# Performance work log

Measured on AMD Instinct MI355X. Metric: run time of the kernel, lower is better.

Reference implementation:

```python
import jax, jax.numpy as jnp
import numpy as np

D = 512
H = 4
HD = D // H
FF = 4 * D
B = 512
T = 128
EMA_K = 128
LOC_K = 4
DECAY = 0.9
STEP = 0.5 / np.sqrt(128 / 32)  # 0.25
EPS = 1e-5


def layernorm(x, g, b):
    mu = jnp.mean(x, axis=-1, keepdims=True)
    var = jnp.mean(jnp.square(x - mu), axis=-1, keepdims=True)
    return (x - mu) * jax.lax.rsqrt(var + EPS) * g + b


def dwconv_causal(x, w):
    # x: (B,T,D), w: (D,K); torch Conv1d(groups=D, padding=K-1) sliced to [:T]
    K = w.shape[1]
    xt = jnp.transpose(x, (0, 2, 1))  # (B,D,T)
    y = jax.lax.conv_general_dilated(
        xt, w[:, None, :], window_strides=(1,), padding=[(K - 1, 0)],
        feature_group_count=x.shape[-1], dimension_numbers=('NCT', 'OIT', 'NCT'))
    return jnp.transpose(y, (0, 2, 1))


def rope(qk, cos, sin):
    # qk: (B,H,T,HD)
    x1, x2 = jnp.split(qk, 2, axis=-1)
    rot = jnp.concatenate([-x2, x1], axis=-1)
    return qk * cos + rot * sin


def setup_inputs() -> dict:
    key = jax.random.key(0)
    ks = jax.random.split(key, 24)
    s = 0.02
    inp = {
        'parallel_repr': jax.random.normal(ks[0], (B, T, D), jnp.float32),
        'sequential_state': jax.random.normal(ks[1], (B, D), jnp.float32),
        'q_w': jax.random.normal(ks[2], (D, D), jnp.float32) * s,
        'q_b': jnp.zeros((D,), jnp.float32),
        'k_w': jax.random.normal(ks[3], (D, D), jnp.float32) * s,
        'k_b': jnp.zeros((D,), jnp.float32),
        'v_w': jax.random.normal(ks[4], (D, D), jnp.float32) * s,
        'v_b': jnp.zeros((D,), jnp.float32),
        'o_w': jax.random.normal(ks[5], (D, D), jnp.float32) * s,
        'o_b': jnp.zeros((D,), jnp.float32),
        'local_w': jax.random.normal(ks[6], (D, LOC_K), jnp.float32) * 0.1,
        'local_b': jax.random.normal(ks[7], (D,), jnp.float32) * 0.1,
        'delta_w': jax.random.normal(ks[8], (3 * D, D), jnp.float32) * s,
        'delta_b': jnp.zeros((D,), jnp.float32),
        'gate_w': jax.random.normal(ks[9], (3 * D, D), jnp.float32) * s,
        'gate_b': jnp.zeros((D,), jnp.float32),
        'dn_g': jnp.ones((D,), jnp.float32), 'dn_b': jnp.zeros((D,), jnp.float32),
        'ln1_g': jnp.ones((D,), jnp.float32), 'ln1_b': jnp.zeros((D,), jnp.float32),
        'ln2_g': jnp.ones((D,), jnp.float32), 'ln2_b': jnp.zeros((D,), jnp.float32),
        'ln3_g': jnp.ones((D,), jnp.float32), 'ln3_b': jnp.zeros((D,), jnp.float32),
        'ln4_g': jnp.ones((D,), jnp.float32), 'ln4_b': jnp.zeros((D,), jnp.float32),
        'seq_w': jax.random.normal(ks[10], (D, D), jnp.float32) * s,
        'seq_b': jnp.zeros((D,), jnp.float32),
        'ffn_w1': jax.random.normal(ks[11], (D, FF), jnp.float32) * s,
        'ffn_b1': jnp.zeros((FF,), jnp.float32),
        'ffn_w2': jax.random.normal(ks[12], (FF, D), jnp.float32) * s,
        'ffn_b2': jnp.zeros((D,), jnp.float32),
    }
    # EMA kernel: coefficient (1-d)*d^lag on x[t-lag]; stored flipped as in torch
    ema = (1.0 - DECAY) * DECAY ** jnp.arange(EMA_K, dtype=jnp.float32)
    inp['ema_w'] = jnp.broadcast_to(ema[::-1][None, :], (D, EMA_K))
    return inp


def reference(parallel_repr, sequential_state, q_w, q_b, k_w, k_b, v_w, v_b,
              o_w, o_b, local_w, local_b, delta_w, delta_b, gate_w, gate_b,
              dn_g, dn_b, ln1_g, ln1_b, ln2_g, ln2_b, ln3_g, ln3_b, ln4_g, ln4_b,
              seq_w, seq_b, ffn_w1, ffn_b1, ffn_w2, ffn_b2, ema_w):
    x = parallel_repr
    Bb, Tt, Dd = x.shape
    # --- RoPE causal attention ---
    inv_freq = 1.0 / (10000.0 ** (jnp.arange(0, HD, 2, dtype=jnp.float32) / HD))
    t = jnp.arange(Tt, dtype=jnp.float32)
    freqs = jnp.outer(t, inv_freq)                      # (T, HD/2)
    emb = jnp.concatenate([freqs, freqs], axis=-1)      # (T, HD)
    cos = jnp.cos(emb)[None, None]
    sin = jnp.sin(emb)[None, None]
    def heads(y):
        return jnp.transpose(y.reshape(Bb, Tt, H, HD), (0, 2, 1, 3))
    q = rope(heads(x @ q_w + q_b), cos, sin)
    k = rope(heads(x @ k_w + k_b), cos, sin)
    v = heads(x @ v_w + v_b)
    scores = jnp.einsum('bhtd,bhsd->bhts', q, k) / np.sqrt(HD)
    causal = jnp.tril(jnp.ones((Tt, Tt), dtype=bool))
    scores = jnp.where(causal, scores, jnp.float32(-1e9))
    attn = jax.nn.softmax(scores, axis=-1)
    attn_out = jnp.einsum('bhts,bhsd->bhtd', attn, v)
    attn_out = jnp.transpose(attn_out, (0, 2, 1, 3)).reshape(Bb, Tt, Dd)
    attn_out = attn_out @ o_w + o_b
    x1 = layernorm(x + attn_out, ln1_g, ln1_b)
    # --- depthwise causal convs ---
    local_hist = dwconv_causal(x1, local_w) + local_b
    global_sum = dwconv_causal(x1, ema_w)
    combined = jnp.concatenate([x1, local_hist, global_sum], axis=-1)  # (B,T,3D)
    deltas = jax.nn.sigmoid(combined @ gate_w + gate_b) * jnp.tanh(combined @ delta_w + delta_b)
    deltas = layernorm(deltas, dn_g, dn_b)
    acc = jnp.cumsum(deltas, axis=1) * STEP
    states = layernorm(sequential_state[:, None, :] + acc, ln3_g, ln3_b)
    seq_guidance = states @ seq_w + seq_b
    ffn_in = x1 + 0.3 * seq_guidance
    h = jax.nn.gelu(ffn_in @ ffn_w1 + ffn_b1, approximate=False)
    ffn_out = h @ ffn_w2 + ffn_b2
    out = layernorm(x1 + ffn_out, ln2_g, ln2_b)
    final_state = layernorm(states[:, -1, :], ln4_g, ln4_b)
    return out, final_state
```

## Files before the change

### kernel.cpp

```cpp
#include <hip/hip_runtime.h>
#include <cstddef>
#include <cstdint>

#define BB   512
#define TT   128
#define DD   512
#define HH   4
#define HDIM 128
#define FFD  2048
#define NROWS (BB * TT)
#define SLOT ((size_t)NROWS * DD)

typedef unsigned short u16;
typedef __bf16 bf16x8 __attribute__((ext_vector_type(8)));
typedef float  f32x4  __attribute__((ext_vector_type(4)));

__device__ __forceinline__ u16 f2b(float x) {
    union { float f; unsigned u; } v; v.f = x;
    unsigned r = v.u + 0x7FFFu + ((v.u >> 16) & 1u);
    return (u16)(r >> 16);
}
__device__ __forceinline__ float b2f(u16 u) {
    union { unsigned u; float f; } v; v.u = (unsigned)u << 16; return v.f;
}

__device__ __forceinline__ void glds16(const void* g, void* l) {
    __builtin_amdgcn_global_load_lds(
        (const __attribute__((address_space(1))) void*)g,
        (__attribute__((address_space(3))) void*)l, 16, 0, 0);
}

template<int MODE>
__global__ __launch_bounds__(256)
void gemm_bf16(const u16* __restrict__ A, const u16* __restrict__ BT,
               const float* __restrict__ bias, void* __restrict__ Cout, int ldc,
               const float* __restrict__ addsrc, int K, int M)
{
    __shared__ u16 As[128 * 32];
    __shared__ u16 Bs[128 * 32];
    __shared__ u16 Ct[(MODE == 5) ? 128 * 128 : 8];
    const int tid = threadIdx.x;
    const int gx  = gridDim.x;
    const int nwg = gx * gridDim.y;
    int orig = blockIdx.y * gx + blockIdx.x;
    if ((nwg & 7) == 0) orig = (orig & 7) * (nwg >> 3) + (orig >> 3);
    const int row0 = (orig / gx) * 128;
    const int col0 = (orig % gx) * 128;

    const int lane = tid & 63;
    const int w    = tid >> 6;
    const int wr   = (w >> 1) * 64;
    const int wc   = (w & 1) * 64;
    const int fr   = lane & 15;
    const int kg   = (lane >> 4) * 8;

    f32x4 acc[4][4];
#pragma unroll
    for (int m = 0; m < 4; ++m)
#pragma unroll
        for (int n = 0; n < 4; ++n) acc[m][n] = (f32x4){0.f, 0.f, 0.f, 0.f};

    const int srow = tid >> 2;
    const int skb  = (tid & 3) * 8;
    const u16* Ag = A  + (size_t)(row0 + srow) * K + skb;
    const u16* Bg = BT + (size_t)(col0 + srow) * K + skb;
    u16* AsP = &As[srow * 32 + skb];
    u16* BsP = &Bs[srow * 32 + skb];

    for (int k0 = 0; k0 < K; k0 += 32) {
        glds16(Ag + k0,                  AsP);
        glds16(Ag + (size_t)64 * K + k0, AsP + 64 * 32);
        glds16(Bg + k0,                  BsP);
        glds16(Bg + (size_t)64 * K + k0, BsP + 64 * 32);
        __syncthreads();
        bf16x8 af[4], bfr[4];
#pragma unroll
        for (int m = 0; m < 4; ++m)
            af[m] = *reinterpret_cast<const bf16x8*>(&As[(wr + m * 16 + fr) * 32 + kg]);
#pragma unroll
        for (int n = 0; n < 4; ++n)
            bfr[n] = *reinterpret_cast<const bf16x8*>(&Bs[(wc + n * 16 + fr) * 32 + kg]);
#pragma unroll
        for (int m = 0; m < 4; ++m)
#pragma unroll
            for (int n = 0; n < 4; ++n)
                acc[m][n] = __builtin_amdgcn_mfma_f32_16x16x32_bf16(af[m], bfr[n], acc[m][n], 0, 0, 0);
        __syncthreads();
    }

    if constexpr (MODE == 5) {
#pragma unroll
        for (int m = 0; m < 4; ++m)
#pragma unroll
            for (int j = 0; j < 4; ++j) {
                const int tl = wr + m * 16 + (lane >> 4) * 4 + j;
#pragma unroll
                for (int n = 0; n < 4; ++n) {
                    const int dc = wc + n * 16 + fr;
                    float v = acc[m][n][j] + bias[col0 + dc];
                    *(u16*)((char*)Ct + dc * 256 + ((tl * 2) ^ ((dc & 7) << 4))) = f2b(v);
                }
            }
        __syncthreads();
        u16* dst = (u16*)Cout + (((size_t)(row0 >> 7) * (M >> 7) + (col0 >> 7)) << 14);
#pragma unroll
        for (int i = 0; i < 8; ++i)
            *(uint4*)(dst + (size_t)(i * 256 + tid) * 8) =
                *(const uint4*)((char*)Ct + (size_t)(i * 256 + tid) * 16);
    } else {
#pragma unroll
        for (int m = 0; m < 4; ++m) {
#pragma unroll
            for (int j = 0; j < 4; ++j) {
                const int r = row0 + wr + m * 16 + (lane >> 4) * 4 + j;
#pragma unroll
                for (int n = 0; n < 4; ++n) {
                    const int c = col0 + wc + n * 16 + fr;
                    float v = acc[m][n][j] + bias[c];
                    if constexpr (MODE == 0) {
                        ((float*)Cout)[(size_t)r * ldc + c] = v;
                    } else if constexpr (MODE == 2) {
                        ((u16*)Cout)[(size_t)r * ldc + c] =
                            f2b(addsrc[(size_t)r * M + c] + 0.3f * v);
                    } else if constexpr (MODE == 3) {
                        float gv = 0.5f * v * (1.f + erff(v * 0.70710678118654752f));
                        ((u16*)Cout)[(size_t)r * ldc + c] = f2b(gv);
                    } else {
                        ((u16*)Cout)[(size_t)r * ldc + c] = f2b(v);
                    }
                }
            }
        }
    }
}

__global__ __launch_bounds__(256)
void wtrans_kernel(const float* __restrict__ W, u16* __restrict__ WT, int K, int M)
{
    __shared__ float t[32][33];
    const int m0 = blockIdx.x * 32;
    const int k0 = blockIdx.y * 32;
    const int tx = threadIdx.x;
    const int ty = threadIdx.y;
#pragma unroll
    for (int i = 0; i < 4; ++i) {
        int k = ty * 4 + i;
        t[k][tx] = W[(size_t)(k0 + k) * M + m0 + tx];
    }
    __syncthreads();
#pragma unroll
    for (int i = 0; i < 4; ++i) {
        int m = ty * 4 + i;
        WT[(size_t)(m0 + m) * K + k0 + tx] = f2b(t[tx][m]);
    }
}

__global__ void cast_f2b_kernel(const float* __restrict__ in, u16* __restrict__ out, size_t n4)
{
    size_t i = (size_t)blockIdx.x * blockDim.x + threadIdx.x;
    if (i >= n4) return;
    float4 v = reinterpret_cast<const float4*>(in)[i];
    union { u16 u[4]; uint2 d; } p;
    p.u[0] = f2b(v.x); p.u[1] = f2b(v.y); p.u[2] = f2b(v.z); p.u[3] = f2b(v.w);
    reinterpret_cast<uint2*>(out)[i] = p.d;
}

__global__ void rope_table_kernel(float* __restrict__ tabc, float* __restrict__ tabs)
{
    int idx = blockIdx.x * blockDim.x + threadIdx.x;
    if (idx >= TT * 64) return;
    int t = idx >> 6, j = idx & 63;
    float invf = expf(-(float)j * (9.210340371976184f / 64.f));
    float ang  = (float)t * invf;
    tabc[idx] = cosf(ang);
    tabs[idx] = sinf(ang);
}

__global__ __launch_bounds__(256)
void attn_mfma_kernel(const u16* __restrict__ Qg, const u16* __restrict__ Kg,
                      const u16* __restrict__ VTg, u16* __restrict__ Og,
                      const float* __restrict__ tabc, const float* __restrict__ tabs)
{
    __shared__ u16 SA[128 * 128];
    __shared__ u16 SB[128 * 128];
    const int h = blockIdx.x, b = blockIdx.y;
    const int tid  = threadIdx.x;
    const int lane = tid & 63;
    const int w    = tid >> 6;
    const int fr   = lane & 15;
    const int kq   = lane >> 4;
    const size_t base = ((size_t)(b * TT)) * DD + (size_t)h * HDIM;

    {
        const int tg = tid >> 4;
        const int dg = tid & 15;
        const int j0 = (dg & 7) * 8;
        const bool hi = (dg & 8) != 0;
        for (int r = 0; r < 8; ++r) {
            const int t = r * 16 + tg;
            uint4 qv = *(const uint4*)(Qg + base + (size_t)t * DD + dg * 8);
            uint4 kv = *(const uint4*)(Kg + base + (size_t)t * DD + dg * 8);
            unsigned qa[4] = {qv.x, qv.y, qv.z, qv.w};
            unsigned ka[4] = {kv.x, kv.y, kv.z, kv.w};
            unsigned qb[4], kb[4];
#pragma unroll
            for (int i = 0; i < 4; ++i) {
                qb[i] = __shfl_xor((int)qa[i], 8);
                kb[i] = __shfl_xor((int)ka[i], 8);
            }
            const float* cp = tabc + t * 64 + j0;
            const float* sp = tabs + t * 64 + j0;
            u16 oq[8], ok[8];
#pragma unroll
            for (int e = 0; e < 8; ++e) {
                float fq = b2f((u16)(qa[e >> 1] >> ((e & 1) * 16)));
                float gq = b2f((u16)(qb[e >> 1] >> ((e & 1) * 16)));
                float fk = b2f((u16)(ka[e >> 1] >> ((e & 1) * 16)));
                float gk = b2f((u16)(kb[e >> 1] >> ((e & 1) * 16)));
                float c = cp[e], s = sp[e];
                oq[e] = f2b(hi ? fq * c + gq * s : fq * c - gq * s);
                ok[e] = f2b(hi ? fk * c + gk * s : fk * c - gk * s);
            }
            const int cb = (dg * 16) ^ ((t & 7) << 4);
            *(uint4*)((char*)SA + t * 256 + cb) = *(const uint4*)oq;
            *(uint4*)((char*)SB + t * 256 + cb) = *(const uint4*)ok;
        }
    }
    __syncthreads();

    f32x4 acc[2][8];
#pragma unroll
    for (int m = 0; m < 2; ++m)
#pragma unroll
        for (int n = 0; n < 8; ++n) acc[m][n] = (f32x4){0.f, 0.f, 0.f, 0.f};

    for (int k0 = 0; k0 < 128; k0 += 32) {
        const int cb = (k0 + kq * 8) * 2;
        bf16x8 af[2];
#pragma unroll
        for (int m = 0; m < 2; ++m) {
            const int row = w * 32 + m * 16 + fr;
            af[m] = *(const bf16x8*)((char*)SA + row * 256 + (cb ^ ((row & 7) << 4)));
        }
#pragma unroll
        for (int n = 0; n < 8; ++n) {
            const int row = n * 16 + fr;
            bf16x8 bf = *(const bf16x8*)((char*)SB + row * 256 + (cb ^ ((row & 7) << 4)));
            acc[0][n] = __builtin_amdgcn_mfma_f32_16x16x32_bf16(af[0], bf, acc[0][n], 0, 0, 0);
            acc[1][n] = __builtin_amdgcn_mfma_f32_16x16x32_bf16(af[1], bf, acc[1][n], 0, 0, 0);
        }
    }
    __syncthreads();

    {
        const u16* vsrc = VTg + ((size_t)(b * HH + h) << 14);
#pragma unroll
        for (int i = 0; i < 8; ++i)
            glds16(vsrc + (size_t)(i * 256 + tid) * 8,
                   SB + (size_t)(i * 256 + tid) * 8);
    }

    const float SC = 0.08838834764831845f;
#pragma unroll
    for (int m = 0; m < 2; ++m) {
#pragma unroll
        for (int j = 0; j < 4; ++j) {
            const int t = w * 32 + m * 16 + kq * 4 + j;
            float mx = -3.0e38f;
#pragma unroll
            for (int n = 0; n < 8; ++n) {
                const int s = n * 16 + fr;
                float v = acc[m][n][j];
                v = (s <= t) ? v * SC : -3.0e38f;
                acc[m][n][j] = v;
                mx = fmaxf(mx, v);
            }
            mx = fmaxf(mx, __shfl_xor(mx, 1));
            mx = fmaxf(mx, __shfl_xor(mx, 2));
            mx = fmaxf(mx, __shfl_xor(mx, 4));
            mx = fmaxf(mx, __shfl_xor(mx, 8));
            float sum = 0.f;
#pragma unroll
            for (int n = 0; n < 8; ++n) {
                float e = __expf(acc[m][n][j] - mx);
                acc[m][n][j] = e; sum += e;
            }
            sum += __shfl_xor(sum, 1); sum += __shfl_xor(sum, 2);
            sum += __shfl_xor(sum, 4); sum += __shfl_xor(sum, 8);
            const float inv = 1.f / sum;
#pragma unroll
            for (int n = 0; n < 8; ++n) {
                const int s = n * 16 + fr;
                *(u16*)((char*)SA + t * 256 + ((s * 2) ^ ((t & 7) << 4))) =
                    f2b(acc[m][n][j] * inv);
            }
        }
    }
    __syncthreads();

    f32x4 oa[2][8];
#pragma unroll
    for (int m = 0; m < 2; ++m)
#pragma unroll
        for (int n = 0; n < 8; ++n) oa[m][n] = (f32x4){0.f, 0.f, 0.f, 0.f};

    for (int k0 = 0; k0 < 128; k0 += 32) {
        const int cb = (k0 + kq * 8) * 2;
        bf16x8 pa[2];
#pragma unroll
        for (int m = 0; m < 2; ++m) {
            const int row = w * 32 + m * 16 + fr;
            pa[m] = *(const bf16x8*)((char*)SA + row * 256 + (cb ^ ((row & 7) << 4)));
        }
#pragma unroll
        for (int n = 0; n < 8; ++n) {
            const int row = n * 16 + fr;
            bf16x8 vb = *(const bf16x8*)((char*)SB + row * 256 + (cb ^ ((row & 7) << 4)));
            oa[0][n] = __builtin_amdgcn_mfma_f32_16x16x32_bf16(pa[0], vb, oa[0][n], 0, 0, 0);
            oa[1][n] = __builtin_amdgcn_mfma_f32_16x16x32_bf16(pa[1], vb, oa[1][n], 0, 0, 0);
        }
    }

#pragma unroll
    for (int m = 0; m < 2; ++m)
#pragma unroll
        for (int j = 0; j < 4; ++j) {
            const int t = w * 32 + m * 16 + kq * 4 + j;
            u16* orow = Og + base + (size_t)t * DD;
#pragma unroll
            for (int n = 0; n < 8; ++n)
                orow[n * 16 + fr] = f2b(oa[m][n][j]);
        }
}

__global__ __launch_bounds__(256)
void ln_kernel(const float* __restrict__ a, size_t a_stride,
               const float* __restrict__ badd, int b_mode,
               const float* __restrict__ g, const float* __restrict__ bb,
               float* __restrict__ out, size_t out_stride,
               u16* __restrict__ out2, size_t out2_stride)
{
    const int row = blockIdx.x;
    const int tid = threadIdx.x;
    const float* ap = a + (size_t)row * a_stride;
    float v0 = ap[tid];
    float v1 = ap[tid + 256];
    if (b_mode == 1) {
        const float* bp = badd + (size_t)row * DD;
        v0 += bp[tid]; v1 += bp[tid + 256];
    } else if (b_mode == 2) {
        const float* bp = badd + (size_t)(row / TT) * DD;
        v0 += bp[tid]; v1 += bp[tid + 256];
    }
    float s  = v0 + v1;
    float ss = v0 * v0 + v1 * v1;
#pragma unroll
    for (int off = 1; off < 64; off <<= 1) {
        s  += __shfl_xor(s, off);
        ss += __shfl_xor(ss, off);
    }
    __shared__ float sm1[4], sm2[4];
    const int wid = tid >> 6;
    if ((tid & 63) == 0) { sm1[wid] = s; sm2[wid] = ss; }
    __syncthreads();
    s  = sm1[0] + sm1[1] + sm1[2] + sm1[3];
    ss = sm2[0] + sm2[1] + sm2[2] + sm2[3];
    const float mu  = s * (1.f / DD);
    const float var = ss * (1.f / DD) - mu * mu;
    const float r   = rsqrtf(var + 1e-5f);
    const float o0 = (v0 - mu) * r * g[tid]       + bb[tid];
    const float o1 = (v1 - mu) * r * g[tid + 256] + bb[tid + 256];
    if (out) {
        float* op = out + (size_t)row * out_stride;
        op[tid] = o0; op[tid + 256] = o1;
    }
    if (out2) {
        u16* op2 = out2 + (size_t)row * out2_stride;
        op2[tid] = f2b(o0); op2[tid + 256] = f2b(o1);
    }
}

__global__ void local_conv_kernel(const float* __restrict__ x, const float* __restrict__ w,
                                  const float* __restrict__ b, u16* __restrict__ y, size_t n)
{
    size_t idx = (size_t)blockIdx.x * blockDim.x + threadIdx.x;
    if (idx >= n) return;
    int d = idx & (DD - 1);
    int t = (int)(idx >> 9) & (TT - 1);
    size_t row = idx >> 9;
    float acc = b[d];
#pragma unroll
    for (int kk = 0; kk < 4; ++kk) {
        int ts = t - 3 + kk;
        if (ts >= 0) acc += w[d * 4 + kk] * x[idx - (size_t)(3 - kk) * DD];
    }
    y[row * 1536 + d] = f2b(acc);
}

__global__ void ema_scan_kernel(const float* __restrict__ x, u16* __restrict__ y)
{
    int idx = blockIdx.x * blockDim.x + threadIdx.x;
    if (idx >= BB * DD) return;
    int b = idx >> 9, d = idx & (DD - 1);
    const float* xp = x + (size_t)b * TT * DD + d;
    u16* yp = y + (size_t)(b * TT) * 1536 + d;
    float acc = 0.f;
    for (int t = 0; t < TT; ++t) {
        acc = 0.9f * acc + 0.1f * xp[(size_t)t * DD];
        yp[(size_t)t * 1536] = f2b(acc);
    }
}

__global__ void cumsum_kernel(const float* __restrict__ x, float* __restrict__ y)
{
    int idx = blockIdx.x * blockDim.x + threadIdx.x;
    if (idx >= BB * DD) return;
    int b = idx >> 9, d = idx & (DD - 1);
    const float* xp = x + (size_t)b * TT * DD + d;
    float* yp = y + (size_t)b * TT * DD + d;
    float acc = 0.f;
    for (int t = 0; t < TT; ++t) {
        acc += xp[(size_t)t * DD];
        yp[(size_t)t * DD] = acc * 0.25f;
    }
}

__global__ void deltas_act_kernel(float* __restrict__ gate, const float* __restrict__ delta,
                                  size_t n)
{
    size_t idx = (size_t)blockIdx.x * blockDim.x + threadIdx.x;
    if (idx >= n) return;
    float gv = gate[idx];
    float dv = delta[idx];
    gate[idx] = (1.f / (1.f + expf(-gv))) * tanhf(dv);
}

extern "C" void kernel_launch(void* const* d_in, const int* in_sizes, int n_in,
                              void* d_out, int out_size, void* d_ws, size_t ws_size,
                              hipStream_t stream)
{
    const float* x       = (const float*)d_in[0];
    const float* seqst   = (const float*)d_in[1];
    const float* q_w     = (const float*)d_in[2];
    const float* q_b     = (const float*)d_in[3];
    const float* k_w     = (const float*)d_in[4];
    const float* k_b     = (const float*)d_in[5];
    const float* v_w     = (const float*)d_in[6];
    const float* v_b     = (const float*)d_in[7];
    const float* o_w     = (const float*)d_in[8];
    const float* o_b     = (const float*)d_in[9];
    const float* local_w = (const float*)d_in[10];
    const float* local_b = (const float*)d_in[11];
    const float* delta_w = (const float*)d_in[12];
    const float* delta_b = (const float*)d_in[13];
    const float* gate_w  = (const float*)d_in[14];
    const float* gate_b  = (const float*)d_in[15];
    const float* dn_g    = (const float*)d_in[16];
    const float* dn_b    = (const float*)d_in[17];
    const float* ln1_g   = (const float*)d_in[18];
    const float* ln1_b   = (const float*)d_in[19];
    const float* ln2_g   = (const float*)d_in[20];
    const float* ln2_b   = (const float*)d_in[21];
    const float* ln3_g   = (const float*)d_in[22];
    const float* ln3_b   = (const float*)d_in[23];
    const float* ln4_g   = (const float*)d_in[24];
    const float* ln4_b   = (const float*)d_in[25];
    const float* seq_w   = (const float*)d_in[26];
    const float* seq_b   = (const float*)d_in[27];
    const float* ffn_w1  = (const float*)d_in[28];
    const float* ffn_b1  = (const float*)d_in[29];
    const float* ffn_w2  = (const float*)d_in[30];
    const float* ffn_b2  = (const float*)d_in[31];
    (void)in_sizes; (void)n_in; (void)out_size; (void)ws_size;

    float* out = (float*)d_out;
    char*  ws  = (char*)d_ws;
    const size_t MB = (size_t)1 << 20;

    u16*   xb   = (u16*)(ws + 0);
    u16*   Qb   = (u16*)(ws + 64 * MB);
    u16*   Kb   = (u16*)(ws + 128 * MB);
    u16*   VTb  = (u16*)(ws + 192 * MB);
    u16*   attnb = (u16*)(ws + 256 * MB);
    u16*   WSa  = (u16*)(ws + 448 * MB);
    u16*   WSb  = (u16*)(ws + 456 * MB);
    float* Oo   = (float*)(ws + 0);
    u16*   Cb   = (u16*)(ws + 128 * MB);
    float* Dl   = (float*)(ws + 320 * MB);
    float* Sst  = Dl;
    u16*   statesb = (u16*)(ws + 0);
    u16*   ffn_inb = (u16*)(ws + 64 * MB);
    u16*   hb      = (u16*)(ws + 128 * MB);
    float* Fo      = (float*)(ws + 0);

    float* X1     = out;
    float* tabc   = out + SLOT;
    float* tabs   = tabc + TT * 64;
    float* fstate = out + SLOT;

    auto wtrans = [&](const float* W, u16* WT, int K, int M) {
        wtrans_kernel<<<dim3(M / 32, K / 32), dim3(32, 8), 0, stream>>>(W, WT, K, M);
    };

    const size_t NE = (size_t)NROWS * DD;
    const int EB = 256;
    const int NBLK = (int)((NE + EB - 1) / EB);

    rope_table_kernel<<<(TT * 64 + 255) / 256, 256, 0, stream>>>(tabc, tabs);
    cast_f2b_kernel<<<(unsigned)((NE / 4 + 255) / 256), 256, 0, stream>>>(x, xb, NE / 4);

    wtrans(q_w, WSa, DD, DD);
    gemm_bf16<4><<<dim3(4, 512), 256, 0, stream>>>(xb, WSa, q_b, Qb, DD, nullptr, DD, DD);
    wtrans(k_w, WSa, DD, DD);
    gemm_bf16<4><<<dim3(4, 512), 256, 0, stream>>>(xb, WSa, k_b, Kb, DD, nullptr, DD, DD);
    wtrans(v_w, WSa, DD, DD);
    gemm_bf16<5><<<dim3(4, 512), 256, 0, stream>>>(xb, WSa, v_b, VTb, 0, nullptr, DD, DD);

    attn_mfma_kernel<<<dim3(HH, BB), 256, 0, stream>>>(Qb, Kb, VTb, attnb, tabc, tabs);

    wtrans(o_w, WSa, DD, DD);
    gemm_bf16<0><<<dim3(4, 512), 256, 0, stream>>>(attnb, WSa, o_b, Oo, DD, nullptr, DD, DD);

    ln_kernel<<<NROWS, 256, 0, stream>>>(x, DD, Oo, 1, ln1_g, ln1_b, X1, DD, Cb, 1536);

    local_conv_kernel<<<NBLK, EB, 0, stream>>>(X1, local_w, local_b, Cb + 512, NE);
    ema_scan_kernel<<<(BB * DD + 255) / 256, 256, 0, stream>>>(X1, Cb + 1024);

    wtrans(gate_w, WSa, 3 * DD, DD);
    gemm_bf16<0><<<dim3(4, 512), 256, 0, stream>>>(Cb, WSa, gate_b, Oo, DD, nullptr, 3 * DD, DD);
    wtrans(delta_w, WSa, 3 * DD, DD);
    gemm_bf16<0><<<dim3(4, 512), 256, 0, stream>>>(Cb, WSa, delta_b, Dl, DD, nullptr, 3 * DD, DD);

    deltas_act_kernel<<<NBLK, EB, 0, stream>>>(Oo, Dl, NE);
    ln_kernel<<<NROWS, 256, 0, stream>>>(Oo, DD, nullptr, 0, dn_g, dn_b, Oo, DD, nullptr, 0);

    cumsum_kernel<<<(BB * DD + 255) / 256, 256, 0, stream>>>(Oo, Sst);
    ln_kernel<<<NROWS, 256, 0, stream>>>(Sst, DD, seqst, 2, ln3_g, ln3_b, Sst, DD, statesb, DD);

    ln_kernel<<<BB, 256, 0, stream>>>(Sst + (size_t)(TT - 1) * DD, (size_t)TT * DD,
                                      nullptr, 0, ln4_g, ln4_b, fstate, DD, nullptr, 0);

    wtrans(seq_w, WSa, DD, DD);
    gemm_bf16<2><<<dim3(4, 512), 256, 0, stream>>>(statesb, WSa, seq_b, ffn_inb, DD, X1, DD, DD);

    wtrans(ffn_w1, WSa, DD, FFD);
    wtrans(ffn_w2, WSb, FFD, DD);
    gemm_bf16<3><<<dim3(16, 512), 256, 0, stream>>>(ffn_inb, WSa, ffn_b1, hb, FFD, nullptr, DD, FFD);
    gemm_bf16<0><<<dim3(4, 512), 256, 0, stream>>>(hb, WSb, ffn_b2, Fo, DD, nullptr, FFD, DD);

    ln_kernel<<<NROWS, 256, 0, stream>>>(X1, DD, Fo, 1, ln2_g, ln2_b, out, DD, nullptr, 0);
}
```

Before: 1.976 ms.

## Fuse QKV and gate/delta GEMMs, double-buffer GEMM, chain LN/conv/scan kernels

```diff
diff --git a/kernel.cpp b/kernel.cpp
--- a/kernel.cpp
+++ b/kernel.cpp
@@ -23,7 +23,12 @@
 __device__ __forceinline__ float b2f(u16 u) {
     union { unsigned u; float f; } v; v.u = (unsigned)u << 16; return v.f;
 }
-
+__device__ __forceinline__ float fast_gelu(float v) {
+    float t = v * (0.7978845608028654f + 0.0356774081f * v * v);
+    float e = __expf(2.f * t);
+    float th = 1.f - 2.f / (e + 1.f);
+    return 0.5f * v * (1.f + th);
+}
 __device__ __forceinline__ void glds16(const void* g, void* l) {
     __builtin_amdgcn_global_load_lds(
         (const __attribute__((address_space(1))) void*)g,
@@ -34,11 +39,10 @@
 __global__ __launch_bounds__(256)
 void gemm_bf16(const u16* __restrict__ A, const u16* __restrict__ BT,
                const float* __restrict__ bias, void* __restrict__ Cout, int ldc,
-               const float* __restrict__ addsrc, int K, int M)
-{
-    __shared__ u16 As[128 * 32];
-    __shared__ u16 Bs[128 * 32];
-    __shared__ u16 Ct[(MODE == 5) ? 128 * 128 : 8];
+               const float* __restrict__ addsrc, void* __restrict__ aux,
+               int K, int M)
+{
+    __shared__ u16 smem[16384];
     const int tid = threadIdx.x;
     const int gx  = gridDim.x;
     const int nwg = gx * gridDim.y;
@@ -64,15 +68,30 @@
     const int skb  = (tid & 3) * 8;
     const u16* Ag = A  + (size_t)(row0 + srow) * K + skb;
     const u16* Bg = BT + (size_t)(col0 + srow) * K + skb;
-    u16* AsP = &As[srow * 32 + skb];
-    u16* BsP = &Bs[srow * 32 + skb];
-
-    for (int k0 = 0; k0 < K; k0 += 32) {
-        glds16(Ag + k0,                  AsP);
-        glds16(Ag + (size_t)64 * K + k0, AsP + 64 * 32);
-        glds16(Bg + k0,                  BsP);
-        glds16(Bg + (size_t)64 * K + k0, BsP + 64 * 32);
+    const int soff = srow * 32 + skb;
+
+    auto stage = [&](int kt, int buf) {
+        const int ko = kt * 32;
+        u16* as = smem + buf * 8192 + soff;
+        u16* bs = smem + buf * 8192 + 4096 + soff;
+        glds16(Ag + ko,                  as);
+        glds16(Ag + (size_t)64 * K + ko, as + 2048);
+        glds16(Bg + ko,                  bs);
+        glds16(Bg + (size_t)64 * K + ko, bs + 2048);
+    };
+
+    const int nk = K >> 5;
+    stage(0, 0);
+    for (int k = 0; k < nk; ++k) {
+        if (k + 1 < nk) {
+            stage(k + 1, (k + 1) & 1);
+            asm volatile("s_waitcnt vmcnt(4)" ::: "memory");
+        } else {
+            asm volatile("s_waitcnt vmcnt(0)" ::: "memory");
+        }
         __syncthreads();
+        const u16* As = smem + (k & 1) * 8192;
+        const u16* Bs = As + 4096;
         bf16x8 af[4], bfr[4];
 #pragma unroll
         for (int m = 0; m < 4; ++m)
@@ -88,25 +107,58 @@
         __syncthreads();
     }
 
-    if constexpr (MODE == 5) {
+    if constexpr (MODE == 7) {
+        if (col0 >= 1024) {
+#pragma unroll
+            for (int m = 0; m < 4; ++m)
+#pragma unroll
+                for (int j = 0; j < 4; ++j) {
+                    const int tl = wr + m * 16 + (lane >> 4) * 4 + j;
+#pragma unroll
+                    for (int n = 0; n < 4; ++n) {
+                        const int dc = wc + n * 16 + fr;
+                        float v = acc[m][n][j] + bias[col0 + dc];
+                        *(u16*)((char*)smem + dc * 256 + ((tl * 2) ^ ((dc & 7) << 4))) = f2b(v);
+                    }
+                }
+            __syncthreads();
+            u16* dst = (u16*)aux + ((size_t)((row0 >> 7) * 4 + ((col0 - 1024) >> 7)) << 14);
+#pragma unroll
+            for (int i = 0; i < 8; ++i)
+                *(uint4*)(dst + (size_t)(i * 256 + tid) * 8) =
+                    *(const uint4*)((char*)smem + (size_t)(i * 256 + tid) * 16);
+        } else {
+#pragma unroll
+            for (int m = 0; m < 4; ++m)
+#pragma unroll
+                for (int j = 0; j < 4; ++j) {
+                    const int r = row0 + wr + m * 16 + (lane >> 4) * 4 + j;
+#pragma unroll
+                    for (int n = 0; n < 4; ++n) {
+                        const int c = col0 + wc + n * 16 + fr;
+                        ((u16*)Cout)[(size_t)r * 1024 + c] = f2b(acc[m][n][j] + bias[c]);
+                    }
+                }
+        }
+    } else if constexpr (MODE == 6) {
 #pragma unroll
         for (int m = 0; m < 4; ++m)
 #pragma unroll
             for (int j = 0; j < 4; ++j) {
-                const int tl = wr + m * 16 + (lane >> 4) * 4 + j;
+                const int r = row0 + wr + m * 16 + (lane >> 4) * 4 + j;
 #pragma unroll
                 for (int n = 0; n < 4; ++n) {
-                    const int dc = wc + n * 16 + fr;
-                    float v = acc[m][n][j] + bias[col0 + dc];
-                    *(u16*)((char*)Ct + dc * 256 + ((tl * 2) ^ ((dc & 7) << 4))) = f2b(v);
+                    const int c = col0 + wc + n * 16 + fr;
+                    float v = acc[m][n][j] + bias[c];
+                    float p = __shfl_xor(v, 1);
+                    if ((fr & 1) == 0) {
+                        float sg = 1.f / (1.f + __expf(-v));
+                        float e  = __expf(2.f * p);
+                        float th = 1.f - 2.f / (e + 1.f);
+                        ((u16*)Cout)[(size_t)r * ldc + (c >> 1)] = f2b(sg * th);
+                    }
                 }
             }
-        __syncthreads();
-        u16* dst = (u16*)Cout + (((size_t)(row0 >> 7) * (M >> 7) + (col0 >> 7)) << 14);
-#pragma unroll
-        for (int i = 0; i < 8; ++i)
-            *(uint4*)(dst + (size_t)(i * 256 + tid) * 8) =
-                *(const uint4*)((char*)Ct + (size_t)(i * 256 + tid) * 16);
     } else {
 #pragma unroll
         for (int m = 0; m < 4; ++m) {
@@ -123,8 +175,7 @@
                         ((u16*)Cout)[(size_t)r * ldc + c] =
                             f2b(addsrc[(size_t)r * M + c] + 0.3f * v);
                     } else if constexpr (MODE == 3) {
-                        float gv = 0.5f * v * (1.f + erff(v * 0.70710678118654752f));
-                        ((u16*)Cout)[(size_t)r * ldc + c] = f2b(gv);
+                        ((u16*)Cout)[(size_t)r * ldc + c] = f2b(fast_gelu(v));
                     } else {
                         ((u16*)Cout)[(size_t)r * ldc + c] = f2b(v);
                     }
@@ -135,7 +186,8 @@
 }
 
 __global__ __launch_bounds__(256)
-void wtrans_kernel(const float* __restrict__ W, u16* __restrict__ WT, int K, int M)
+void wtrans_kernel(const float* __restrict__ W, u16* __restrict__ WT, int K, int M,
+                   int rmul, int roff)
 {
     __shared__ float t[32][33];
     const int m0 = blockIdx.x * 32;
@@ -151,7 +203,7 @@
 #pragma unroll
     for (int i = 0; i < 4; ++i) {
         int m = ty * 4 + i;
-        WT[(size_t)(m0 + m) * K + k0 + tx] = f2b(t[tx][m]);
+        WT[(size_t)((m0 + m) * rmul + roff) * K + k0 + tx] = f2b(t[tx][m]);
     }
 }
 
@@ -176,9 +228,19 @@
     tabs[idx] = sinf(ang);
 }
 
+__global__ void bias_build_kernel(const float* qb, const float* kb, const float* vb,
+                                  const float* gb, const float* db,
+                                  float* qkvb, float* gdb)
+{
+    int i = blockIdx.x * blockDim.x + threadIdx.x;
+    if (i >= 512) return;
+    qkvb[i] = qb[i]; qkvb[512 + i] = kb[i]; qkvb[1024 + i] = vb[i];
+    gdb[2 * i] = gb[i]; gdb[2 * i + 1] = db[i];
+}
+
 __global__ __launch_bounds__(256)
-void attn_mfma_kernel(const u16* __restrict__ Qg, const u16* __restrict__ Kg,
-                      const u16* __restrict__ VTg, u16* __restrict__ Og,
+void attn_mfma_kernel(const u16* __restrict__ QKg, const u16* __restrict__ VTg,
+                      u16* __restrict__ Og,
                       const float* __restrict__ tabc, const float* __restrict__ tabs)
 {
     __shared__ u16 SA[128 * 128];
@@ -189,7 +251,8 @@
     const int w    = tid >> 6;
     const int fr   = lane & 15;
     const int kq   = lane >> 4;
-    const size_t base = ((size_t)(b * TT)) * DD + (size_t)h * HDIM;
+    const size_t baseq = ((size_t)(b * TT)) * 1024 + (size_t)h * HDIM;
+    const size_t baseo = ((size_t)(b * TT)) * DD + (size_t)h * HDIM;
 
     {
         const int tg = tid >> 4;
@@ -198,8 +261,8 @@
         const bool hi = (dg & 8) != 0;
         for (int r = 0; r < 8; ++r) {
             const int t = r * 16 + tg;
-            uint4 qv = *(const uint4*)(Qg + base + (size_t)t * DD + dg * 8);
-            uint4 kv = *(const uint4*)(Kg + base + (size_t)t * DD + dg * 8);
+            uint4 qv = *(const uint4*)(QKg + baseq + (size_t)t * 1024 + dg * 8);
+            uint4 kv = *(const uint4*)(QKg + baseq + 512 + (size_t)t * 1024 + dg * 8);
             unsigned qa[4] = {qv.x, qv.y, qv.z, qv.w};
             unsigned ka[4] = {kv.x, kv.y, kv.z, kv.w};
             unsigned qb[4], kb[4];
@@ -326,32 +389,112 @@
 #pragma unroll
         for (int j = 0; j < 4; ++j) {
             const int t = w * 32 + m * 16 + kq * 4 + j;
-            u16* orow = Og + base + (size_t)t * DD;
+            u16* orow = Og + baseo + (size_t)t * DD;
 #pragma unroll
             for (int n = 0; n < 8; ++n)
                 orow[n * 16 + fr] = f2b(oa[m][n][j]);
         }
 }
 
+__device__ __forceinline__ float2 blk_red512(float v, float (*red)[2], int tid)
+{
+    float s = v, ss = v * v;
+#pragma unroll
+    for (int off = 1; off < 64; off <<= 1) {
+        s  += __shfl_xor(s, off);
+        ss += __shfl_xor(ss, off);
+    }
+    if ((tid & 63) == 0) { red[tid >> 6][0] = s; red[tid >> 6][1] = ss; }
+    __syncthreads();
+    float S = 0.f, SS = 0.f;
+#pragma unroll
+    for (int w = 0; w < 8; ++w) { S += red[w][0]; SS += red[w][1]; }
+    return make_float2(S, SS);
+}
+
+__global__ __launch_bounds__(512)
+void ln1_chain_kernel(const float* __restrict__ x, const u16* __restrict__ oo,
+                      const float* __restrict__ g, const float* __restrict__ bb,
+                      const float* __restrict__ lw, const float* __restrict__ lb,
+                      float* __restrict__ X1, u16* __restrict__ Cb)
+{
+    __shared__ float red[2][8][2];
+    const int b = blockIdx.x, d = threadIdx.x;
+    const float g_ = g[d], b_ = bb[d];
+    const float w0 = lw[d * 4 + 0], w1 = lw[d * 4 + 1],
+                w2 = lw[d * 4 + 2], w3 = lw[d * 4 + 3];
+    const float lb_ = lb[d];
+    const size_t rb = (size_t)b * TT;
+    float h1 = 0.f, h2 = 0.f, h3 = 0.f, ema = 0.f;
+    float v = x[(rb + 0) * DD + d] + b2f(oo[(rb + 0) * DD + d]);
+    for (int t = 0; t < TT; ++t) {
+        const int tn = (t < TT - 1) ? t + 1 : t;
+        float vn = x[(rb + tn) * DD + d] + b2f(oo[(rb + tn) * DD + d]);
+        float2 r = blk_red512(v, red[t & 1], d);
+        float mu  = r.x * (1.f / DD);
+        float var = r.y * (1.f / DD) - mu * mu;
+        float x1v = (v - mu) * rsqrtf(var + 1e-5f) * g_ + b_;
+        const size_t row = rb + t;
+        X1[row * DD + d] = x1v;
+        u16* crow = Cb + row * 1536;
+        crow[d] = f2b(x1v);
+        crow[512 + d]  = f2b(lb_ + w3 * x1v + w2 * h1 + w1 * h2 + w0 * h3);
+        ema = 0.9f * ema + 0.1f * x1v;
+        crow[1024 + d] = f2b(ema);
+        h3 = h2; h2 = h1; h1 = x1v;
+        v = vn;
+    }
+}
+
+__global__ __launch_bounds__(512)
+void state_chain_kernel(const u16* __restrict__ deltasB, const float* __restrict__ seqst,
+                        const float* __restrict__ dng, const float* __restrict__ dnb,
+                        const float* __restrict__ g3, const float* __restrict__ b3,
+                        const float* __restrict__ g4, const float* __restrict__ b4,
+                        u16* __restrict__ statesb, float* __restrict__ fstate)
+{
+    __shared__ float red[2][8][2];
+    const int b = blockIdx.x, d = threadIdx.x;
+    const float gd_ = dng[d], bd_ = dnb[d], g3_ = g3[d], b3_ = b3[d];
+    const float seq = seqst[(size_t)b * DD + d];
+    const size_t rb = (size_t)b * TT;
+    float cum = 0.f;
+    float v = b2f(deltasB[(rb + 0) * DD + d]);
+    for (int t = 0; t < TT; ++t) {
+        const int tn = (t < TT - 1) ? t + 1 : t;
+        float vn = b2f(deltasB[(rb + tn) * DD + d]);
+        float2 r0 = blk_red512(v, red[0], d);
+        float mu  = r0.x * (1.f / DD);
+        float var = r0.y * (1.f / DD) - mu * mu;
+        float nd  = (v - mu) * rsqrtf(var + 1e-5f) * gd_ + bd_;
+        cum += nd;
+        float sv = seq + cum * 0.25f;
+        float2 r1 = blk_red512(sv, red[1], d);
+        mu  = r1.x * (1.f / DD);
+        var = r1.y * (1.f / DD) - mu * mu;
+        float o = (sv - mu) * rsqrtf(var + 1e-5f) * g3_ + b3_;
+        statesb[(rb + t) * DD + d] = f2b(o);
+        if (t == TT - 1) {
+            float2 r2 = blk_red512(o, red[0], d);
+            float mu4  = r2.x * (1.f / DD);
+            float var4 = r2.y * (1.f / DD) - mu4 * mu4;
+            fstate[(size_t)b * DD + d] = (o - mu4) * rsqrtf(var4 + 1e-5f) * g4[d] + b4[d];
+        }
+        v = vn;
+    }
+}
+
 __global__ __launch_bounds__(256)
-void ln_kernel(const float* __restrict__ a, size_t a_stride,
-               const float* __restrict__ badd, int b_mode,
-               const float* __restrict__ g, const float* __restrict__ bb,
-               float* __restrict__ out, size_t out_stride,
-               u16* __restrict__ out2, size_t out2_stride)
+void ln2_kernel(const float* __restrict__ a, const u16* __restrict__ badd,
+                const float* __restrict__ g, const float* __restrict__ bb,
+                float* __restrict__ out)
 {
     const int row = blockIdx.x;
     const int tid = threadIdx.x;
-    const float* ap = a + (size_t)row * a_stride;
-    float v0 = ap[tid];
-    float v1 = ap[tid + 256];
-    if (b_mode == 1) {
-        const float* bp = badd + (size_t)row * DD;
-        v0 += bp[tid]; v1 += bp[tid + 256];
-    } else if (b_mode == 2) {
-        const float* bp = badd + (size_t)(row / TT) * DD;
-        v0 += bp[tid]; v1 += bp[tid + 256];
-    }
+    const float* ap = a + (size_t)row * DD;
+    const u16*   bp = badd + (size_t)row * DD;
+    float v0 = ap[tid]       + b2f(bp[tid]);
+    float v1 = ap[tid + 256] + b2f(bp[tid + 256]);
     float s  = v0 + v1;
     float ss = v0 * v0 + v1 * v1;
 #pragma unroll
@@ -368,71 +511,9 @@
     const float mu  = s * (1.f / DD);
     const float var = ss * (1.f / DD) - mu * mu;
     const float r   = rsqrtf(var + 1e-5f);
-    const float o0 = (v0 - mu) * r * g[tid]       + bb[tid];
-    const float o1 = (v1 - mu) * r * g[tid + 256] + bb[tid + 256];
-    if (out) {
-        float* op = out + (size_t)row * out_stride;
-        op[tid] = o0; op[tid + 256] = o1;
-    }
-    if (out2) {
-        u16* op2 = out2 + (size_t)row * out2_stride;
-        op2[tid] = f2b(o0); op2[tid + 256] = f2b(o1);
-    }
-}
-
-__global__ void local_conv_kernel(const float* __restrict__ x, const float* __restrict__ w,
-                                  const float* __restrict__ b, u16* __restrict__ y, size_t n)
-{
-    size_t idx = (size_t)blockIdx.x * blockDim.x + threadIdx.x;
-    if (idx >= n) return;
-    int d = idx & (DD - 1);
-    int t = (int)(idx >> 9) & (TT - 1);
-    size_t row = idx >> 9;
-    float acc = b[d];
-#pragma unroll
-    for (int kk = 0; kk < 4; ++kk) {
-        int ts = t - 3 + kk;
-        if (ts >= 0) acc += w[d * 4 + kk] * x[idx - (size_t)(3 - kk) * DD];
-    }
-    y[row * 1536 + d] = f2b(acc);
-}
-
-__global__ void ema_scan_kernel(const float* __restrict__ x, u16* __restrict__ y)
-{
-    int idx = blockIdx.x * blockDim.x + threadIdx.x;
-    if (idx >= BB * DD) return;
-    int b = idx >> 9, d = idx & (DD - 1);
-    const float* xp = x + (size_t)b * TT * DD + d;
-    u16* yp = y + (size_t)(b * TT) * 1536 + d;
-    float acc = 0.f;
-    for (int t = 0; t < TT; ++t) {
-        acc = 0.9f * acc + 0.1f * xp[(size_t)t * DD];
-        yp[(size_t)t * 1536] = f2b(acc);
-    }
-}
-
-__global__ void cumsum_kernel(const float* __restrict__ x, float* __restrict__ y)
-{
-    int idx = blockIdx.x * blockDim.x + threadIdx.x;
-    if (idx >= BB * DD) return;
-    int b = idx >> 9, d = idx & (DD - 1);
-    const float* xp = x + (size_t)b * TT * DD + d;
-    float* yp = y + (size_t)b * TT * DD + d;
-    float acc = 0.f;
-    for (int t = 0; t < TT; ++t) {
-        acc += xp[(size_t)t * DD];
-        yp[(size_t)t * DD] = acc * 0.25f;
-    }
-}
-
-__global__ void deltas_act_kernel(float* __restrict__ gate, const float* __restrict__ delta,
-                                  size_t n)
-{
-    size_t idx = (size_t)blockIdx.x * blockDim.x + threadIdx.x;
-    if (idx >= n) return;
-    float gv = gate[idx];
-    float dv = delta[idx];
-    gate[idx] = (1.f / (1.f + expf(-gv))) * tanhf(dv);
+    float* op = out + (size_t)row * DD;
+    op[tid]       = (v0 - mu) * r * g[tid]       + bb[tid];
+    op[tid + 256] = (v1 - mu) * r * g[tid + 256] + bb[tid + 256];
 }
 
 extern "C" void kernel_launch(void* const* d_in, const int* in_sizes, int n_in,
@@ -477,76 +558,72 @@
     char*  ws  = (char*)d_ws;
     const size_t MB = (size_t)1 << 20;
 
-    u16*   xb   = (u16*)(ws + 0);
-    u16*   Qb   = (u16*)(ws + 64 * MB);
-    u16*   Kb   = (u16*)(ws + 128 * MB);
-    u16*   VTb  = (u16*)(ws + 192 * MB);
-    u16*   attnb = (u16*)(ws + 256 * MB);
-    u16*   WSa  = (u16*)(ws + 448 * MB);
-    u16*   WSb  = (u16*)(ws + 456 * MB);
-    float* Oo   = (float*)(ws + 0);
-    u16*   Cb   = (u16*)(ws + 128 * MB);
-    float* Dl   = (float*)(ws + 320 * MB);
-    float* Sst  = Dl;
-    u16*   statesb = (u16*)(ws + 0);
-    u16*   ffn_inb = (u16*)(ws + 64 * MB);
-    u16*   hb      = (u16*)(ws + 128 * MB);
-    float* Fo      = (float*)(ws + 0);
+    u16*   xb      = (u16*)(ws + 0);
+    u16*   QKb     = (u16*)(ws + 64 * MB);
+    u16*   VTb     = (u16*)(ws + 192 * MB);
+    u16*   attnb   = (u16*)(ws + 256 * MB);
+    u16*   Oob     = (u16*)(ws + 0);
+    u16*   Cb      = (u16*)(ws + 64 * MB);
+    u16*   deltasB = (u16*)(ws + 256 * MB);
+    u16*   statesb = (u16*)(ws + 320 * MB);
+    u16*   ffn_inb = (u16*)(ws + 0);
+    u16*   hb      = (u16*)(ws + 64 * MB);
+    u16*   Fob     = (u16*)(ws + 320 * MB);
+    u16*   WSq  = (u16*)(ws + 448 * MB);
+    u16*   WSo  = (u16*)(ws + 450 * MB);
+    u16*   WSgd = (u16*)(ws + 451 * MB);
+    u16*   WSs  = (u16*)(ws + 455 * MB);
+    u16*   WSf1 = (u16*)(ws + 456 * MB);
+    u16*   WSf2 = (u16*)(ws + 458 * MB);
+    float* qkvb = (float*)(ws + 460 * MB);
+    float* gdb  = (float*)(ws + 461 * MB);
 
     float* X1     = out;
     float* tabc   = out + SLOT;
     float* tabs   = tabc + TT * 64;
     float* fstate = out + SLOT;
 
-    auto wtrans = [&](const float* W, u16* WT, int K, int M) {
-        wtrans_kernel<<<dim3(M / 32, K / 32), dim3(32, 8), 0, stream>>>(W, WT, K, M);
-    };
-
     const size_t NE = (size_t)NROWS * DD;
-    const int EB = 256;
-    const int NBLK = (int)((NE + EB - 1) / EB);
 
     rope_table_kernel<<<(TT * 64 + 255) / 256, 256, 0, stream>>>(tabc, tabs);
     cast_f2b_kernel<<<(unsigned)((NE / 4 + 255) / 256), 256, 0, stream>>>(x, xb, NE / 4);
-
-    wtrans(q_w, WSa, DD, DD);
-    gemm_bf16<4><<<dim3(4, 512), 256, 0, stream>>>(xb, WSa, q_b, Qb, DD, nullptr, DD, DD);
-    wtrans(k_w, WSa, DD, DD);
-    gemm_bf16<4><<<dim3(4, 512), 256, 0, stream>>>(xb, WSa, k_b, Kb, DD, nullptr, DD, DD);
-    wtrans(v_w, WSa, DD, DD);
-    gemm_bf16<5><<<dim3(4, 512), 256, 0, stream>>>(xb, WSa, v_b, VTb, 0, nullptr, DD, DD);
-
-    attn_mfma_kernel<<<dim3(HH, BB), 256, 0, stream>>>(Qb, Kb, VTb, attnb, tabc, tabs);
-
-    wtrans(o_w, WSa, DD, DD);
-    gemm_bf16<0><<<dim3(4, 512), 256, 0, stream>>>(attnb, WSa, o_b, Oo, DD, nullptr, DD, DD);
-
-    ln_kernel<<<NROWS, 256, 0, stream>>>(x, DD, Oo, 1, ln1_g, ln1_b, X1, DD, Cb, 1536);
-
-    local_conv_kernel<<<NBLK, EB, 0, stream>>>(X1, local_w, local_b, Cb + 512, NE);
-    ema_scan_kernel<<<(BB * DD + 255) / 256, 256, 0, stream>>>(X1, Cb + 1024);
-
-    wtrans(gate_w, WSa, 3 * DD, DD);
-    gemm_bf16<0><<<dim3(4, 512), 256, 0, stream>>>(Cb, WSa, gate_b, Oo, DD, nullptr, 3 * DD, DD);
-    wtrans(delta_w, WSa, 3 * DD, DD);
-    gemm_bf16<0><<<dim3(4, 512), 256, 0, stream>>>(Cb, WSa, delta_b, Dl, DD, nullptr, 3 * DD, DD);
-
-    deltas_act_kernel<<<NBLK, EB, 0, stream>>>(Oo, Dl, NE);
-    ln_kernel<<<NROWS, 256, 0, stream>>>(Oo, DD, nullptr, 0, dn_g, dn_b, Oo, DD, nullptr, 0);
-
-    cumsum_kernel<<<(BB * DD + 255) / 256, 256, 0, stream>>>(Oo, Sst);
-    ln_kernel<<<NROWS, 256, 0, stream>>>(Sst, DD, seqst, 2, ln3_g, ln3_b, Sst, DD, statesb, DD);
-
-    ln_kernel<<<BB, 256, 0, stream>>>(Sst + (size_t)(TT - 1) * DD, (size_t)TT * DD,
-                                      nullptr, 0, ln4_g, ln4_b, fstate, DD, nullptr, 0);
-
-    wtrans(seq_w, WSa, DD, DD);
-    gemm_bf16<2><<<dim3(4, 512), 256, 0, stream>>>(statesb, WSa, seq_b, ffn_inb, DD, X1, DD, DD);
-
-    wtrans(ffn_w1, WSa, DD, FFD);
-    wtrans(ffn_w2, WSb, FFD, DD);
-    gemm_bf16<3><<<dim3(16, 512), 256, 0, stream>>>(ffn_inb, WSa, ffn_b1, hb, FFD, nullptr, DD, FFD);
-    gemm_bf16<0><<<dim3(4, 512), 256, 0, stream>>>(hb, WSb, ffn_b2, Fo, DD, nullptr, FFD, DD);
-
-    ln_kernel<<<NROWS, 256, 0, stream>>>(X1, DD, Fo, 1, ln2_g, ln2_b, out, DD, nullptr, 0);
-}
+    bias_build_kernel<<<2, 256, 0, stream>>>(q_b, k_b, v_b, gate_b, delta_b, qkvb, gdb);
+    auto wt = [&](const float* W, u16* WT, int K, int M, int rmul, int roff) {
+        wtrans_kernel<<<dim3(M / 32, K / 32), dim3(32, 8), 0, stream>>>(W, WT, K, M, rmul, roff);
+    };
+    wt(q_w, WSq, DD, DD, 1, 0);
+    wt(k_w, WSq + (size_t)512 * DD, DD, DD, 1, 0);
+    wt(v_w, WSq + (size_t)1024 * DD, DD, DD, 1, 0);
+    wt(o_w, WSo, DD, DD, 1, 0);
+    wt(gate_w,  WSgd, 3 * DD, DD, 2, 0);
+    wt(delta_w, WSgd, 3 * DD, DD, 2, 1);
+    wt(seq_w, WSs, DD, DD, 1, 0);
+    wt(ffn_w1, WSf1, DD, FFD, 1, 0);
+    wt(ffn_w2, WSf2, FFD, DD, 1, 0);
+
+    gemm_bf16<7><<<dim3(12, 512), 256, 0, stream>>>(
+        xb, WSq, qkvb, QKb, 1024, nullptr, VTb, DD, 1536);
+
+    attn_mfma_kernel<<<dim3(HH, BB), 256, 0, stream>>>(QKb, VTb, attnb, tabc, tabs);
+
+    gemm_bf16<4><<<dim3(4, 512), 256, 0, stream>>>(
+        attnb, WSo, o_b, Oob, DD, nullptr, nullptr, DD, DD);
+
+    ln1_chain_kernel<<<BB, 512, 0, stream>>>(x, Oob, ln1_g, ln1_b, local_w, local_b, X1, Cb);
+
+    gemm_bf16<6><<<dim3(8, 512), 256, 0, stream>>>(
+        Cb, WSgd, gdb, deltasB, DD, nullptr, nullptr, 3 * DD, 1024);
+
+    state_chain_kernel<<<BB, 512, 0, stream>>>(
+        deltasB, seqst, dn_g, dn_b, ln3_g, ln3_b, ln4_g, ln4_b, statesb, fstate);
+
+    gemm_bf16<2><<<dim3(4, 512), 256, 0, stream>>>(
+        statesb, WSs, seq_b, ffn_inb, DD, X1, nullptr, DD, DD);
+
+    gemm_bf16<3><<<dim3(16, 512), 256, 0, stream>>>(
+        ffn_inb, WSf1, ffn_b1, hb, FFD, nullptr, nullptr, DD, FFD);
+    gemm_bf16<4><<<dim3(4, 512), 256, 0, stream>>>(
+        hb, WSf2, ffn_b2, Fob, DD, nullptr, nullptr, FFD, DD);
+
+    ln2_kernel<<<NROWS, 256, 0, stream>>>(X1, Fob, ln2_g, ln2_b, out);
+}
```

Result: faster. 1.770 ms (-10.4%).
